# Kernel tuning notes

Hardware: AMD Instinct MI355X
Metric: run time of the kernel (lower is better)

The kernel has to match this reference:

```python
import jax, jax.numpy as jnp
import numpy as np

N_NODES = 100000
N_EDGES = 1600000
F_IN = 64
C = 128          # hidden_encoding == element_embedding
STEPS = 4
NEG_SLOPE = 0.01  # torch.nn.LeakyReLU default


def setup_inputs() -> dict:
    key = jax.random.key(0)
    ks = jax.random.split(key, 8)
    s = 0.05
    return {
        "x": jax.random.normal(ks[0], (N_NODES, F_IN), dtype=jnp.float32),
        "edge_index": jax.random.randint(ks[1], (2, N_EDGES), 0, N_NODES, dtype=jnp.int64),
        "W_in": jax.random.normal(ks[2], (C, F_IN), dtype=jnp.float32) * s,
        "W_mpnn": jax.random.normal(ks[3], (STEPS, C, C), dtype=jnp.float32) * s,
        "W_ih": jax.random.normal(ks[4], (3 * C, C), dtype=jnp.float32) * s,
        "W_hh": jax.random.normal(ks[5], (3 * C, C), dtype=jnp.float32) * s,
        "b_ih": jnp.zeros((3 * C,), dtype=jnp.float32),
        "b_hh": jnp.zeros((3 * C,), dtype=jnp.float32),
        "W_pred": jax.random.normal(ks[6], (1, C), dtype=jnp.float32) * s,
        "b_pred": jnp.zeros((1,), dtype=jnp.float32),
    }


def reference(x, edge_index, W_in, W_mpnn, W_ih, W_hh, b_ih, b_hh, W_pred, b_pred):
    src, dst = edge_index[0], edge_index[1]
    n = x.shape[0]
    # input embedding (bias=False)
    h = x @ W_in.T                                  # [N, C]
    for i in range(STEPS):
        m = h @ W_mpnn[i]                           # [N, C] (PyG: matmul(x, weight[i]))
        agg = jax.ops.segment_sum(m[src], dst, num_segments=n)  # scatter-add aggr
        # torch GRUCell, gate order r, z, n
        gi = agg @ W_ih.T + b_ih                    # [N, 3C]
        gh = h @ W_hh.T + b_hh                      # [N, 3C]
        r = jax.nn.sigmoid(gi[:, :C] + gh[:, :C])
        z = jax.nn.sigmoid(gi[:, C:2 * C] + gh[:, C:2 * C])
        nn_ = jnp.tanh(gi[:, 2 * C:] + r * gh[:, 2 * C:])
        h = (1.0 - z) * nn_ + z * h
    h = jnp.where(h >= 0, h, NEG_SLOPE * h)         # LeakyReLU
    g = jnp.mean(h, axis=0)                         # graph readout [C]
    return g @ W_pred.T + b_pred                    # [1]
```

## Files before the change

### kernel.cpp

```cpp
#include <hip/hip_runtime.h>
#include <cstdint>

typedef __attribute__((ext_vector_type(8))) short bf16x8;
typedef __attribute__((ext_vector_type(4))) float f32x4;
typedef __attribute__((address_space(1))) unsigned int ga_u32;
typedef __attribute__((address_space(3))) unsigned int ls_u32;

__device__ __forceinline__ float bf2f(unsigned short u) {
    union { unsigned int i; float f; } v; v.i = ((unsigned int)u) << 16; return v.f;
}
__device__ __forceinline__ float bfhi(unsigned int w) {
    union { unsigned int i; float f; } v; v.i = w & 0xffff0000u; return v.f;
}
__device__ __forceinline__ float bflo(unsigned int w) {
    union { unsigned int i; float f; } v; v.i = w << 16; return v.f;
}
__device__ __forceinline__ unsigned short f2bf(float f) {
    union { float ff; unsigned int i; } v; v.ff = f;
    unsigned int r = (v.i + 0x7fffu + ((v.i >> 16) & 1u)) >> 16;
    return (unsigned short)r;
}
__device__ __forceinline__ int origcol(int nc) {
    int w = nc / 96, rem = nc % 96, g = rem / 32, cc = rem % 32;
    return g * 128 + w * 32 + cc;
}

__global__ void detect_kernel(const unsigned int* __restrict__ x32,
                              const int* __restrict__ ei32,
                              int* __restrict__ flags)
{
    __shared__ int insaneS;
    __shared__ int orS;
    int tid = threadIdx.x;
    if (tid == 0) { insaneS = 0; orS = 0; }
    __syncthreads();
    int insane = 0;
    for (int j = tid; j < 512; j += 256) {
        unsigned int w = x32[j];
        int e = (int)((w >> 7) & 0xFF);
        if (e > 135 || e < 100) insane++;
    }
    int ov = 0;
    for (int j = tid; j < 256; j += 256) ov |= ei32[2 * j + 1];
    atomicAdd(&insaneS, insane);
    atomicOr(&orS, ov);
    __syncthreads();
    if (tid == 0) {
        flags[0] = (insaneS < 64) ? 1 : 0;
        flags[1] = (orS == 0) ? 1 : 0;
    }
}

__global__ void convall_kernel(const void* W_in, const void* W_mpnn, const void* W_ih,
                               const void* W_hh, const void* b_ih, const void* b_hh,
                               const void* W_pred, const void* b_pred,
                               float* __restrict__ Winf, float* __restrict__ Wmf,
                               float* __restrict__ Wihf, float* __restrict__ Whhf,
                               float* __restrict__ bihf, float* __restrict__ bhhf,
                               float* __restrict__ Wpf, float* __restrict__ bpf,
                               int steps, const int* __restrict__ flags)
{
    int i = blockIdx.x * 256 + threadIdx.x;
    int bf = flags[0];
    auto get = [&](const void* p, int idx) -> float {
        return bf ? bf2f(((const unsigned short*)p)[idx]) : ((const float*)p)[idx];
    };
    int n0 = 8192, n1 = n0 + steps * 16384, n2 = n1 + 49152, n3 = n2 + 49152;
    int n4 = n3 + 384, n5 = n4 + 384, n6 = n5 + 128, n7 = n6 + 1;
    if      (i < n0) Winf[i]      = get(W_in,   i);
    else if (i < n1) Wmf[i - n0]  = get(W_mpnn, i - n0);
    else if (i < n2) Wihf[i - n1] = get(W_ih,   i - n1);
    else if (i < n3) Whhf[i - n2] = get(W_hh,   i - n2);
    else if (i < n4) bihf[i - n3] = get(b_ih,   i - n3);
    else if (i < n5) bhhf[i - n4] = get(b_hh,   i - n4);
    else if (i < n6) Wpf[i - n5]  = get(W_pred, i - n5);
    else if (i < n7) bpf[i - n6]  = get(b_pred, i - n6);
}

__global__ void wcomb_kernel(const float* __restrict__ Wm,
                             const float* __restrict__ Wih,
                             float* __restrict__ Wcomb, int steps)
{
    int i = blockIdx.x * 256 + threadIdx.x;
    int total = steps * 49152;
    if (i >= total) return;
    int step = i / 49152;
    int rem = i - step * 49152;
    int k = rem / 384;
    int j = rem - k * 384;
    const float* wm = Wm + ((long)step * 128 + k) * 128;
    const float* wi = Wih + (long)j * 128;
    float s = 0.f;
#pragma unroll 8
    for (int t = 0; t < 128; ++t) s += wm[t] * wi[t];
    Wcomb[i] = s;
}

__global__ void pack_gates(const float* __restrict__ Wcomb,
                           const float* __restrict__ Whhf,
                           const float* __restrict__ bihf, const float* __restrict__ bhhf,
                           unsigned short* __restrict__ Bci,
                           unsigned short* __restrict__ Bhh,
                           float* __restrict__ bip, float* __restrict__ bhp,
                           int steps)
{
    int i = blockIdx.x * 256 + threadIdx.x;
    int nmat = steps * 49152;
    if (i < nmat) {
        int s = i / 49152, r = i - s * 49152;
        int t = r >> 11, rem = r & 2047;
        int ks = rem >> 9, l = (rem >> 3) & 63, j = rem & 7;
        int k = ks * 32 + (l >> 4) * 8 + j;
        int oc = origcol(t * 16 + (l & 15));
        Bci[i] = f2bf(Wcomb[(long)s * 49152 + k * 384 + oc]);
    } else if (i < nmat + 49152) {
        int r = i - nmat;
        int t = r >> 11, rem = r & 2047;
        int ks = rem >> 9, l = (rem >> 3) & 63, j = rem & 7;
        int k = ks * 32 + (l >> 4) * 8 + j;
        int oc = origcol(t * 16 + (l & 15));
        Bhh[r] = f2bf(Whhf[(long)oc * 128 + k]);
    } else if (i < nmat + 49152 + 768) {
        int b = i - nmat - 49152;
        if (b < 384) bip[b] = bihf[origcol(b)];
        else         bhp[b - 384] = bhhf[origcol(b - 384)];
    }
}

__global__ void pack_in(const float* __restrict__ Winf, unsigned short* __restrict__ Bin)
{
    int r = blockIdx.x * 256 + threadIdx.x;
    if (r >= 8192) return;
    int t = r >> 10, rem = r & 1023;
    int ks = rem >> 9, l = (rem >> 3) & 63, j = rem & 7;
    int k = ks * 32 + (l >> 4) * 8 + j;
    int col = t * 16 + (l & 15);
    Bin[r] = f2bf(Winf[col * 64 + k]);
}

__global__ __launch_bounds__(256) void gemm_in(const void* __restrict__ xraw,
                        const int* __restrict__ flags,
                        const unsigned short* __restrict__ Bin,
                        unsigned short* __restrict__ hout, int N)
{
    const int w = threadIdx.x >> 6, lane = threadIdx.x & 63;
    const int m = lane & 15, quad = lane >> 4;
    const int rowBase = blockIdx.x * 32;
    const bool abf = flags[0] != 0;
    f32x4 acc[2][2];
#pragma unroll
    for (int rt = 0; rt < 2; ++rt)
#pragma unroll
        for (int ct = 0; ct < 2; ++ct) acc[rt][ct] = (f32x4){0.f, 0.f, 0.f, 0.f};

#pragma unroll
    for (int ks = 0; ks < 2; ++ks) {
        bf16x8 a[2];
#pragma unroll
        for (int rt = 0; rt < 2; ++rt) {
            long row = rowBase + rt * 16 + m;
            if (abf) {
                a[rt] = *(const bf16x8*)(const void*)((const unsigned short*)xraw + row * 64 + ks * 32 + quad * 8);
            } else {
                const float* xp = (const float*)xraw + row * 64 + ks * 32 + quad * 8;
                float4 f0 = *(const float4*)xp;
                float4 f1 = *(const float4*)(xp + 4);
                bf16x8 t;
                t[0] = (short)f2bf(f0.x); t[1] = (short)f2bf(f0.y);
                t[2] = (short)f2bf(f0.z); t[3] = (short)f2bf(f0.w);
                t[4] = (short)f2bf(f1.x); t[5] = (short)f2bf(f1.y);
                t[6] = (short)f2bf(f1.z); t[7] = (short)f2bf(f1.w);
                a[rt] = t;
            }
        }
#pragma unroll
        for (int ct = 0; ct < 2; ++ct) {
            int t = w * 2 + ct;
            bf16x8 b = *(const bf16x8*)(const void*)(Bin + ((t * 2 + ks) * 64 + lane) * 8);
#pragma unroll
            for (int rt = 0; rt < 2; ++rt)
                acc[rt][ct] = __builtin_amdgcn_mfma_f32_16x16x32_bf16(a[rt], b, acc[rt][ct], 0, 0, 0);
        }
    }
#pragma unroll
    for (int rt = 0; rt < 2; ++rt)
#pragma unroll
        for (int ct = 0; ct < 2; ++ct)
#pragma unroll
            for (int reg = 0; reg < 4; ++reg) {
                int row = rowBase + rt * 16 + quad * 4 + reg;
                int col = w * 32 + ct * 16 + m;
                if (row < N) hout[(long)row * 128 + col] = f2bf(acc[rt][ct][reg]);
            }
}

__global__ __launch_bounds__(512, 2) void step_kernel(
    const unsigned short* __restrict__ hin,
    const unsigned short* __restrict__ aggb,
    const unsigned short* __restrict__ Bci,
    const unsigned short* __restrict__ Bhh,
    const float* __restrict__ bip, const float* __restrict__ bhp,
    unsigned short* __restrict__ hout, int N)
{
    __shared__ unsigned short lds[8192];
    const int tid = threadIdx.x;
    const int w = tid >> 6, lane = tid & 63;
    const int m = lane & 15, quad = lane >> 4;
    const int cg = w >> 1, half = w & 1;
    const long rowBase = (long)blockIdx.x * 32;
    const int col = cg * 32 + half * 16 + m;

    {
        int lrow = w * 4 + (lane >> 4);
        int schunk = (lane & 15) ^ (lrow & 7);
        const unsigned short* gap = aggb + (rowBase + lrow) * 128 + schunk * 8;
        const unsigned short* ghp = hin  + (rowBase + lrow) * 128 + schunk * 8;
        ls_u32* la = (ls_u32*)(lds + w * 512);
        ls_u32* lh = (ls_u32*)(lds + 4096 + w * 512);
        __builtin_amdgcn_global_load_lds((const ga_u32*)gap, la, 16, 0, 0);
        __builtin_amdgcn_global_load_lds((const ga_u32*)ghp, lh, 16, 0, 0);
    }

    bf16x8 bI[4][3], bH[4][3];
#pragma unroll
    for (int ks = 0; ks < 4; ++ks)
#pragma unroll
        for (int g = 0; g < 3; ++g) {
            int t = cg * 6 + g * 2 + half;
            bI[ks][g] = *(const bf16x8*)(const void*)(Bci + (((long)t * 4 + ks) * 64 + lane) * 8);
            bH[ks][g] = *(const bf16x8*)(const void*)(Bhh + (((long)t * 4 + ks) * 64 + lane) * 8);
        }

    f32x4 gi[2][3], gh[2][3];
#pragma unroll
    for (int g = 0; g < 3; ++g) {
        int nc = (cg * 6 + g * 2 + half) * 16 + m;
        float bi = bip[nc], bh = bhp[nc];
#pragma unroll
        for (int rt = 0; rt < 2; ++rt) {
            gi[rt][g] = (f32x4){bi, bi, bi, bi};
            gh[rt][g] = (f32x4){bh, bh, bh, bh};
        }
    }

    __syncthreads();

#pragma unroll
    for (int ks = 0; ks < 4; ++ks) {
        bf16x8 aA[2], hA[2];
#pragma unroll
        for (int rt = 0; rt < 2; ++rt) {
            int r = rt * 16 + m;
            int ch = (ks * 4 + quad) ^ (r & 7);
            aA[rt] = *(const bf16x8*)(const void*)(lds + r * 128 + ch * 8);
            hA[rt] = *(const bf16x8*)(const void*)(lds + 4096 + r * 128 + ch * 8);
        }
#pragma unroll
        for (int g = 0; g < 3; ++g)
#pragma unroll
            for (int rt = 0; rt < 2; ++rt) {
                gi[rt][g] = __builtin_amdgcn_mfma_f32_16x16x32_bf16(aA[rt], bI[ks][g], gi[rt][g], 0, 0, 0);
                gh[rt][g] = __builtin_amdgcn_mfma_f32_16x16x32_bf16(hA[rt], bH[ks][g], gh[rt][g], 0, 0, 0);
            }
    }

#pragma unroll
    for (int rt = 0; rt < 2; ++rt)
#pragma unroll
        for (int reg = 0; reg < 4; ++reg) {
            long row = rowBase + rt * 16 + quad * 4 + reg;
            if (row < N) {
                int r2 = rt * 16 + quad * 4 + reg;
                int hidx = r2 * 128 + ((((col >> 3) ^ (r2 & 7)) << 3) + (col & 7));
                float R  = __builtin_amdgcn_rcpf(1.f + __expf(-(gi[rt][0][reg] + gh[rt][0][reg])));
                float Z  = __builtin_amdgcn_rcpf(1.f + __expf(-(gi[rt][1][reg] + gh[rt][1][reg])));
                float u  = gi[rt][2][reg] + R * gh[rt][2][reg];
                float e2 = __expf(-2.f * fabsf(u));
                float Nn = copysignf((1.f - e2) * __builtin_amdgcn_rcpf(1.f + e2), u);
                float hold = bf2f(lds[4096 + hidx]);
                hout[row * 128 + col] = f2bf((1.f - Z) * Nn + Z * hold);
            }
        }
}

__global__ __launch_bounds__(256) void part1_kernel(
    const int* __restrict__ ei, int E, const int* __restrict__ flags,
    int* __restrict__ gcnt, uint2* __restrict__ pair2,
    int nb, int cshift, int ccap, int chunk)
{
    __shared__ int cnt[256];
    __shared__ int base_s[256];
    const int tid = threadIdx.x;
    if (tid < nb) cnt[tid] = 0;
    __syncthreads();
    const bool i64 = flags[1] != 0;
    const long long* e64 = (const long long*)ei;
    int lo = blockIdx.x * chunk;
    int hi = lo + chunk; if (hi > E) hi = E;
    for (int i = lo + tid; i < hi; i += 256) {
        int d = i64 ? (int)e64[(long)E + i] : ei[(long)E + i];
        atomicAdd(&cnt[d >> cshift], 1);
    }
    __syncthreads();
    if (tid < nb) {
        int c = cnt[tid];
        base_s[tid] = (c > 0) ? atomicAdd(&gcnt[tid], c) : 0;
        cnt[tid] = 0;
    }
    __syncthreads();
    for (int i = lo + tid; i < hi; i += 256) {
        int s, d;
        if (i64) { s = (int)e64[i]; d = (int)e64[(long)E + i]; }
        else     { s = ei[i];       d = ei[(long)E + i]; }
        int c = d >> cshift;
        int p = base_s[c] + atomicAdd(&cnt[c], 1);
        if (p < ccap) { uint2 pr; pr.x = (unsigned)s; pr.y = (unsigned)d; pair2[(long)c * ccap + p] = pr; }
    }
}

__global__ void scanco_kernel(const int* __restrict__ gcnt, int* __restrict__ cbase,
                              int nb, int ccap)
{
    __shared__ int wsum[4];
    int tid = threadIdx.x, lane = tid & 63, wv = tid >> 6;
    int x = (tid < nb) ? gcnt[tid] : 0;
    if (x > ccap) x = ccap;
    int inc = x;
#pragma unroll
    for (int d = 1; d < 64; d <<= 1) { int u = __shfl_up(inc, d); if (lane >= d) inc += u; }
    if (lane == 63) wsum[wv] = inc;
    __syncthreads();
    if (tid == 0) { int s = 0; for (int q = 0; q < 4; ++q) { int t = wsum[q]; wsum[q] = s; s += t; } }
    __syncthreads();
    int excl = wsum[wv] + inc - x;
    if (tid < nb) cbase[tid] = excl;
    if (tid == nb - 1) cbase[nb] = excl + x;
}

__global__ __launch_bounds__(256) void part2_kernel(
    const uint2* __restrict__ pair2, const int* __restrict__ gcnt,
    const int* __restrict__ cbase,
    int* __restrict__ offs, int* __restrict__ csr,
    int N, int nb, int cshift, int ccap)
{
    __shared__ int lb[2048];
    __shared__ int wsum[4];
    const int b = blockIdx.x, tid = threadIdx.x;
    const int span = 1 << cshift;
    const int n0 = b << cshift;
    int count = gcnt[b]; if (count > ccap) count = ccap;
    for (int k = tid; k < span; k += 256) lb[k] = 0;
    __syncthreads();
    const uint2* pp = pair2 + (long)b * ccap;
    for (int i = tid; i < count; i += 256)
        atomicAdd(&lb[(int)pp[i].y - n0], 1);
    __syncthreads();
    int npe = span >> 8; if (npe < 1) npe = 1;
    int myb = tid * npe;
    int vals[8];
    int sum = 0;
    for (int k = 0; k < npe; ++k) { vals[k] = lb[myb + k]; sum += vals[k]; }
    int lane = tid & 63, wv = tid >> 6;
    int inc = sum;
#pragma unroll
    for (int d = 1; d < 64; d <<= 1) { int u = __shfl_up(inc, d); if (lane >= d) inc += u; }
    if (lane == 63) wsum[wv] = inc;
    __syncthreads();
    if (tid == 0) { int s = 0; for (int q = 0; q < 4; ++q) { int t = wsum[q]; wsum[q] = s; s += t; } }
    __syncthreads();
    int run = wsum[wv] + inc - sum;
    __syncthreads();
    for (int k = 0; k < npe; ++k) { lb[myb + k] = run; run += vals[k]; }
    __syncthreads();
    int gb = cbase[b];
    int nn = N - n0; if (nn > span) nn = span;
    for (int g = tid; g < nn; g += 256) offs[n0 + g] = gb + lb[g];
    if (b == nb - 1 && tid == 0) offs[N] = cbase[nb];
    __syncthreads();
    for (int i = tid; i < count; i += 256) {
        uint2 pr = pp[i];
        int p = gb + atomicAdd(&lb[(int)pr.y - n0], 1);
        csr[p] = (int)pr.x;
    }
}

__global__ __launch_bounds__(256) void aggregate(const unsigned short* __restrict__ hb,
                          const int* __restrict__ off,
                          const int* __restrict__ csr,
                          unsigned short* __restrict__ aggb, int n)
{
    int wv = threadIdx.x >> 6, lane = threadIdx.x & 63;
    int slot = lane >> 4;
    int c16 = lane & 15;
    int nw = gridDim.x * 4;
    int wid = blockIdx.x * 4 + wv;
    int chunk = (n + nw - 1) / nw;
    int lo = wid * chunk;
    int hi = lo + chunk; if (hi > n) hi = n;

    for (int node = lo; node < hi; ++node) {
        int s0 = off[node], s1 = off[node + 1];
        float a0 = 0.f, a1 = 0.f, a2 = 0.f, a3 = 0.f, a4 = 0.f, a5 = 0.f, a6 = 0.f, a7 = 0.f;
        if (s1 > s0) {
            int last = s1 - 1;
            for (int j = s0 + slot; j < s1; j += 16) {
                uint4 vv[4];
                float wt[4];
#pragma unroll
                for (int t = 0; t < 4; ++t) {
                    int jj = j + 4 * t;
                    int idx = csr[jj <= last ? jj : last];
                    vv[t] = *(const uint4*)(const void*)(hb + (long)idx * 128 + c16 * 8);
                    wt[t] = (jj <= last) ? 1.f : 0.f;
                }
#pragma unroll
                for (int t = 0; t < 4; ++t) {
                    a0 = fmaf(bflo(vv[t].x), wt[t], a0);
                    a1 = fmaf(bfhi(vv[t].x), wt[t], a1);
                    a2 = fmaf(bflo(vv[t].y), wt[t], a2);
                    a3 = fmaf(bfhi(vv[t].y), wt[t], a3);
                    a4 = fmaf(bflo(vv[t].z), wt[t], a4);
                    a5 = fmaf(bfhi(vv[t].z), wt[t], a5);
                    a6 = fmaf(bflo(vv[t].w), wt[t], a6);
                    a7 = fmaf(bfhi(vv[t].w), wt[t], a7);
                }
            }
        }
        a0 += __shfl_xor(a0, 16); a1 += __shfl_xor(a1, 16);
        a2 += __shfl_xor(a2, 16); a3 += __shfl_xor(a3, 16);
        a4 += __shfl_xor(a4, 16); a5 += __shfl_xor(a5, 16);
        a6 += __shfl_xor(a6, 16); a7 += __shfl_xor(a7, 16);
        a0 += __shfl_xor(a0, 32); a1 += __shfl_xor(a1, 32);
        a2 += __shfl_xor(a2, 32); a3 += __shfl_xor(a3, 32);
        a4 += __shfl_xor(a4, 32); a5 += __shfl_xor(a5, 32);
        a6 += __shfl_xor(a6, 32); a7 += __shfl_xor(a7, 32);
        if (slot == 0) {
            uint4 o;
            o.x = ((unsigned int)f2bf(a1) << 16) | f2bf(a0);
            o.y = ((unsigned int)f2bf(a3) << 16) | f2bf(a2);
            o.z = ((unsigned int)f2bf(a5) << 16) | f2bf(a4);
            o.w = ((unsigned int)f2bf(a7) << 16) | f2bf(a6);
            *(uint4*)(void*)(aggb + (long)node * 128 + c16 * 8) = o;
        }
    }
}

__global__ void colsum(const unsigned short* __restrict__ hb, float* __restrict__ acc, int n) {
    int c = threadIdx.x & 127;
    int sub = threadIdx.x >> 7;
    float local = 0.f;
    for (long r = blockIdx.x * 2 + sub; r < n; r += (long)gridDim.x * 2) {
        float v = bf2f(hb[r * 128 + c]);
        local += (v >= 0.f) ? v : 0.01f * v;
    }
    atomicAdd(&acc[c], local);
}

__global__ void finalize(const float* __restrict__ acc,
                         const float* __restrict__ W_pred_f,
                         const float* __restrict__ b_pred_f,
                         unsigned int* __restrict__ out, float invN)
{
    __shared__ float ws2[2];
    int t = threadIdx.x;
    float v = acc[t] * invN * W_pred_f[t];
#pragma unroll
    for (int d = 32; d >= 1; d >>= 1) v += __shfl_down(v, d);
    if ((t & 63) == 0) ws2[t >> 6] = v;
    __syncthreads();
    if (t == 0) {
        float r = ws2[0] + ws2[1] + b_pred_f[0];
        unsigned int bf = (unsigned int)f2bf(r);
        out[0] = (bf << 16) | bf;
    }
}

extern "C" void kernel_launch(void* const* d_in, const int* in_sizes, int n_in,
                              void* d_out, int out_size, void* d_ws, size_t ws_size,
                              hipStream_t stream)
{
    const void* x      = d_in[0];
    const int*  ei     = (const int*)d_in[1];
    const void* W_in   = d_in[2];
    const void* W_mpnn = d_in[3];
    const void* W_ih   = d_in[4];
    const void* W_hh   = d_in[5];
    const void* b_ih   = d_in[6];
    const void* b_hh   = d_in[7];
    const void* W_pred = d_in[8];
    const void* b_pred = d_in[9];

    const int N = in_sizes[0] / 64;
    const int E = in_sizes[1] / 2;
    const int STEPS = in_sizes[3] / (128 * 128);

    int cshift = 9;
    while ((((N + (1 << cshift) - 1) >> cshift)) > 256 && cshift < 11) cshift++;
    const int NCO = (N + (1 << cshift) - 1) >> cshift;
    const int ccap = (((E / NCO) * 3 / 2 + 1024) + 255) & ~255;
    const int chunk = (E + 255) / 256;

    size_t woff = 0;
    auto carve = [&](size_t bytes) -> void* {
        void* p = (char*)d_ws + woff;
        woff = (woff + bytes + 255) & ~(size_t)255;
        return p;
    };
    int*   flags = (int*)carve(2 * 4);
    float* Winf  = (float*)carve(8192 * 4);
    float* Wmf   = (float*)carve((size_t)STEPS * 16384 * 4);
    float* Wihf  = (float*)carve(49152 * 4);
    float* Whhf  = (float*)carve(49152 * 4);
    float* bihf  = (float*)carve(384 * 4);
    float* bhhf  = (float*)carve(384 * 4);
    float* Wpf   = (float*)carve(128 * 4);
    float* bpf   = (float*)carve(4);
    float* Wcomb = (float*)carve((size_t)STEPS * 49152 * 4);
    unsigned short* Bci = (unsigned short*)carve((size_t)STEPS * 49152 * 2);
    unsigned short* Bhh = (unsigned short*)carve(49152 * 2);
    unsigned short* Bin = (unsigned short*)carve(8192 * 2);
    float* bip   = (float*)carve(384 * 4);
    float* bhp   = (float*)carve(384 * 4);
    unsigned short* hA   = (unsigned short*)carve(((size_t)N * 128 + 16384) * 2);
    unsigned short* hB   = (unsigned short*)carve(((size_t)N * 128 + 16384) * 2);
    unsigned short* aggb = (unsigned short*)carve(((size_t)N * 128 + 16384) * 2);
    int*   gcnt  = (int*)carve(256 * 4);
    int*   cbase = (int*)carve(257 * 4);
    int*   offs  = (int*)carve((size_t)(N + 1) * 4);
    int*   csr   = (int*)carve((size_t)E * 4 + 256);
    uint2* pair2 = (uint2*)carve((size_t)NCO * ccap * 8);
    float* accb  = (float*)carve(128 * 4);

    hipMemsetAsync(gcnt, 0, 256 * 4, stream);
    hipMemsetAsync(accb, 0, 128 * 4, stream);

    detect_kernel<<<1, 256, 0, stream>>>((const unsigned int*)x, ei, flags);

    {
        int total = 8192 + STEPS * 16384 + 2 * 49152 + 768 + 129;
        convall_kernel<<<(total + 255) / 256, 256, 0, stream>>>(
            W_in, W_mpnn, W_ih, W_hh, b_ih, b_hh, W_pred, b_pred,
            Winf, Wmf, Wihf, Whhf, bihf, bhhf, Wpf, bpf, STEPS, flags);
    }

    wcomb_kernel<<<(STEPS * 49152 + 255) / 256, 256, 0, stream>>>(Wmf, Wihf, Wcomb, STEPS);
    {
        int total = (STEPS + 1) * 49152 + 768;
        pack_gates<<<(total + 255) / 256, 256, 0, stream>>>(Wcomb, Whhf, bihf, bhhf,
                                                            Bci, Bhh, bip, bhp, STEPS);
    }
    pack_in<<<32, 256, 0, stream>>>(Winf, Bin);

    gemm_in<<<(N + 31) / 32, 256, 0, stream>>>(x, flags, Bin, hA, N);

    part1_kernel<<<256, 256, 0, stream>>>(ei, E, flags, gcnt, pair2, NCO, cshift, ccap, chunk);
    scanco_kernel<<<1, 256, 0, stream>>>(gcnt, cbase, NCO, ccap);
    part2_kernel<<<NCO, 256, 0, stream>>>(pair2, gcnt, cbase, offs, csr, N, NCO, cshift, ccap);

    int aggBlocks = (N + 3) / 4; if (aggBlocks > 2048) aggBlocks = 2048;
    unsigned short* hcur = hA;
    unsigned short* hnxt = hB;
    for (int step = 0; step < STEPS; ++step) {
        aggregate<<<aggBlocks, 256, 0, stream>>>(hcur, offs, csr, aggb, N);
        step_kernel<<<(N + 31) / 32, 512, 0, stream>>>(
            hcur, aggb, Bci + (size_t)step * 49152, Bhh, bip, bhp, hnxt, N);
        unsigned short* t = hcur; hcur = hnxt; hnxt = t;
    }

    colsum<<<512, 256, 0, stream>>>(hcur, accb, N);
    finalize<<<1, 128, 0, stream>>>(accb, Wpf, bpf, (unsigned int*)d_out, 1.f / (float)N);
}
```

Measured before the change: 678.4 us.

## Fuse neighbor aggregation into GRU step kernel via LDS staging

Merges the separate aggregate kernel into the per-step GRU kernel. Each 512-thread block gathers and sums neighbor rows for its 32 nodes (4 rows per wave) and writes the bf16 result straight into swizzled LDS, so the aggregate buffer is neither written to nor read back from global memory. This also removes one kernel launch per step. In exchange, the gather work is now split into fixed 32-node tiles with less load balancing, and its latency may not overlap well with the MFMA phase.

```diff
diff --git a/kernel.cpp b/kernel.cpp
--- a/kernel.cpp
+++ b/kernel.cpp
@@ -194,9 +194,10 @@
             }
 }
 
-__global__ __launch_bounds__(512, 2) void step_kernel(
+__global__ __launch_bounds__(512, 2) void fused_step(
     const unsigned short* __restrict__ hin,
-    const unsigned short* __restrict__ aggb,
+    const int* __restrict__ off,
+    const int* __restrict__ csr,
     const unsigned short* __restrict__ Bci,
     const unsigned short* __restrict__ Bhh,
     const float* __restrict__ bip, const float* __restrict__ bhp,
@@ -209,220 +210,48 @@
     const int cg = w >> 1, half = w & 1;
     const long rowBase = (long)blockIdx.x * 32;
     const int col = cg * 32 + half * 16 + m;
+    const int slot = lane >> 4;
+    const int c16 = lane & 15;
 
     {
-        int lrow = w * 4 + (lane >> 4);
-        int schunk = (lane & 15) ^ (lrow & 7);
-        const unsigned short* gap = aggb + (rowBase + lrow) * 128 + schunk * 8;
-        const unsigned short* ghp = hin  + (rowBase + lrow) * 128 + schunk * 8;
-        ls_u32* la = (ls_u32*)(lds + w * 512);
+        int lrow = w * 4 + slot;
+        int schunk = c16 ^ (lrow & 7);
+        const unsigned short* ghp = hin + (rowBase + lrow) * 128 + schunk * 8;
         ls_u32* lh = (ls_u32*)(lds + 4096 + w * 512);
-        __builtin_amdgcn_global_load_lds((const ga_u32*)gap, la, 16, 0, 0);
         __builtin_amdgcn_global_load_lds((const ga_u32*)ghp, lh, 16, 0, 0);
     }
 
-    bf16x8 bI[4][3], bH[4][3];
-#pragma unroll
-    for (int ks = 0; ks < 4; ++ks)
-#pragma unroll
-        for (int g = 0; g < 3; ++g) {
-            int t = cg * 6 + g * 2 + half;
-            bI[ks][g] = *(const bf16x8*)(const void*)(Bci + (((long)t * 4 + ks) * 64 + lane) * 8);
-            bH[ks][g] = *(const bf16x8*)(const void*)(Bhh + (((long)t * 4 + ks) * 64 + lane) * 8);
-        }
-
-    f32x4 gi[2][3], gh[2][3];
-#pragma unroll
-    for (int g = 0; g < 3; ++g) {
-        int nc = (cg * 6 + g * 2 + half) * 16 + m;
-        float bi = bip[nc], bh = bhp[nc];
-#pragma unroll
-        for (int rt = 0; rt < 2; ++rt) {
-            gi[rt][g] = (f32x4){bi, bi, bi, bi};
-            gh[rt][g] = (f32x4){bh, bh, bh, bh};
-        }
-    }
-
-    __syncthreads();
-
-#pragma unroll
-    for (int ks = 0; ks < 4; ++ks) {
-        bf16x8 aA[2], hA[2];
-#pragma unroll
-        for (int rt = 0; rt < 2; ++rt) {
-            int r = rt * 16 + m;
-            int ch = (ks * 4 + quad) ^ (r & 7);
-            aA[rt] = *(const bf16x8*)(const void*)(lds + r * 128 + ch * 8);
-            hA[rt] = *(const bf16x8*)(const void*)(lds + 4096 + r * 128 + ch * 8);
-        }
-#pragma unroll
-        for (int g = 0; g < 3; ++g)
-#pragma unroll
-            for (int rt = 0; rt < 2; ++rt) {
-                gi[rt][g] = __builtin_amdgcn_mfma_f32_16x16x32_bf16(aA[rt], bI[ks][g], gi[rt][g], 0, 0, 0);
-                gh[rt][g] = __builtin_amdgcn_mfma_f32_16x16x32_bf16(hA[rt], bH[ks][g], gh[rt][g], 0, 0, 0);
-            }
-    }
-
-#pragma unroll
-    for (int rt = 0; rt < 2; ++rt)
-#pragma unroll
-        for (int reg = 0; reg < 4; ++reg) {
-            long row = rowBase + rt * 16 + quad * 4 + reg;
-            if (row < N) {
-                int r2 = rt * 16 + quad * 4 + reg;
-                int hidx = r2 * 128 + ((((col >> 3) ^ (r2 & 7)) << 3) + (col & 7));
-                float R  = __builtin_amdgcn_rcpf(1.f + __expf(-(gi[rt][0][reg] + gh[rt][0][reg])));
-                float Z  = __builtin_amdgcn_rcpf(1.f + __expf(-(gi[rt][1][reg] + gh[rt][1][reg])));
-                float u  = gi[rt][2][reg] + R * gh[rt][2][reg];
-                float e2 = __expf(-2.f * fabsf(u));
-                float Nn = copysignf((1.f - e2) * __builtin_amdgcn_rcpf(1.f + e2), u);
-                float hold = bf2f(lds[4096 + hidx]);
-                hout[row * 128 + col] = f2bf((1.f - Z) * Nn + Z * hold);
-            }
-        }
-}
-
-__global__ __launch_bounds__(256) void part1_kernel(
-    const int* __restrict__ ei, int E, const int* __restrict__ flags,
-    int* __restrict__ gcnt, uint2* __restrict__ pair2,
-    int nb, int cshift, int ccap, int chunk)
-{
-    __shared__ int cnt[256];
-    __shared__ int base_s[256];
-    const int tid = threadIdx.x;
-    if (tid < nb) cnt[tid] = 0;
-    __syncthreads();
-    const bool i64 = flags[1] != 0;
-    const long long* e64 = (const long long*)ei;
-    int lo = blockIdx.x * chunk;
-    int hi = lo + chunk; if (hi > E) hi = E;
-    for (int i = lo + tid; i < hi; i += 256) {
-        int d = i64 ? (int)e64[(long)E + i] : ei[(long)E + i];
-        atomicAdd(&cnt[d >> cshift], 1);
-    }
-    __syncthreads();
-    if (tid < nb) {
-        int c = cnt[tid];
-        base_s[tid] = (c > 0) ? atomicAdd(&gcnt[tid], c) : 0;
-        cnt[tid] = 0;
-    }
-    __syncthreads();
-    for (int i = lo + tid; i < hi; i += 256) {
-        int s, d;
-        if (i64) { s = (int)e64[i]; d = (int)e64[(long)E + i]; }
-        else     { s = ei[i];       d = ei[(long)E + i]; }
-        int c = d >> cshift;
-        int p = base_s[c] + atomicAdd(&cnt[c], 1);
-        if (p < ccap) { uint2 pr; pr.x = (unsigned)s; pr.y = (unsigned)d; pair2[(long)c * ccap + p] = pr; }
-    }
-}
-
-__global__ void scanco_kernel(const int* __restrict__ gcnt, int* __restrict__ cbase,
-                              int nb, int ccap)
-{
-    __shared__ int wsum[4];
-    int tid = threadIdx.x, lane = tid & 63, wv = tid >> 6;
-    int x = (tid < nb) ? gcnt[tid] : 0;
-    if (x > ccap) x = ccap;
-    int inc = x;
-#pragma unroll
-    for (int d = 1; d < 64; d <<= 1) { int u = __shfl_up(inc, d); if (lane >= d) inc += u; }
-    if (lane == 63) wsum[wv] = inc;
-    __syncthreads();
-    if (tid == 0) { int s = 0; for (int q = 0; q < 4; ++q) { int t = wsum[q]; wsum[q] = s; s += t; } }
-    __syncthreads();
-    int excl = wsum[wv] + inc - x;
-    if (tid < nb) cbase[tid] = excl;
-    if (tid == nb - 1) cbase[nb] = excl + x;
-}
-
-__global__ __launch_bounds__(256) void part2_kernel(
-    const uint2* __restrict__ pair2, const int* __restrict__ gcnt,
-    const int* __restrict__ cbase,
-    int* __restrict__ offs, int* __restrict__ csr,
-    int N, int nb, int cshift, int ccap)
-{
-    __shared__ int lb[2048];
-    __shared__ int wsum[4];
-    const int b = blockIdx.x, tid = threadIdx.x;
-    const int span = 1 << cshift;
-    const int n0 = b << cshift;
-    int count = gcnt[b]; if (count > ccap) count = ccap;
-    for (int k = tid; k < span; k += 256) lb[k] = 0;
-    __syncthreads();
-    const uint2* pp = pair2 + (long)b * ccap;
-    for (int i = tid; i < count; i += 256)
-        atomicAdd(&lb[(int)pp[i].y - n0], 1);
-    __syncthreads();
-    int npe = span >> 8; if (npe < 1) npe = 1;
-    int myb = tid * npe;
-    int vals[8];
-    int sum = 0;
-    for (int k = 0; k < npe; ++k) { vals[k] = lb[myb + k]; sum += vals[k]; }
-    int lane = tid & 63, wv = tid >> 6;
-    int inc = sum;
-#pragma unroll
-    for (int d = 1; d < 64; d <<= 1) { int u = __shfl_up(inc, d); if (lane >= d) inc += u; }
-    if (lane == 63) wsum[wv] = inc;
-    __syncthreads();
-    if (tid == 0) { int s = 0; for (int q = 0; q < 4; ++q) { int t = wsum[q]; wsum[q] = s; s += t; } }
-    __syncthreads();
-    int run = wsum[wv] + inc - sum;
-    __syncthreads();
-    for (int k = 0; k < npe; ++k) { lb[myb + k] = run; run += vals[k]; }
-    __syncthreads();
-    int gb = cbase[b];
-    int nn = N - n0; if (nn > span) nn = span;
-    for (int g = tid; g < nn; g += 256) offs[n0 + g] = gb + lb[g];
-    if (b == nb - 1 && tid == 0) offs[N] = cbase[nb];
-    __syncthreads();
-    for (int i = tid; i < count; i += 256) {
-        uint2 pr = pp[i];
-        int p = gb + atomicAdd(&lb[(int)pr.y - n0], 1);
-        csr[p] = (int)pr.x;
-    }
-}
-
-__global__ __launch_bounds__(256) void aggregate(const unsigned short* __restrict__ hb,
-                          const int* __restrict__ off,
-                          const int* __restrict__ csr,
-                          unsigned short* __restrict__ aggb, int n)
-{
-    int wv = threadIdx.x >> 6, lane = threadIdx.x & 63;
-    int slot = lane >> 4;
-    int c16 = lane & 15;
-    int nw = gridDim.x * 4;
-    int wid = blockIdx.x * 4 + wv;
-    int chunk = (n + nw - 1) / nw;
-    int lo = wid * chunk;
-    int hi = lo + chunk; if (hi > n) hi = n;
-
-    for (int node = lo; node < hi; ++node) {
-        int s0 = off[node], s1 = off[node + 1];
-        float a0 = 0.f, a1 = 0.f, a2 = 0.f, a3 = 0.f, a4 = 0.f, a5 = 0.f, a6 = 0.f, a7 = 0.f;
-        if (s1 > s0) {
-            int last = s1 - 1;
-            for (int j = s0 + slot; j < s1; j += 16) {
-                uint4 vv[4];
-                float wt[4];
-#pragma unroll
-                for (int t = 0; t < 4; ++t) {
-                    int jj = j + 4 * t;
-                    int idx = csr[jj <= last ? jj : last];
-                    vv[t] = *(const uint4*)(const void*)(hb + (long)idx * 128 + c16 * 8);
-                    wt[t] = (jj <= last) ? 1.f : 0.f;
-                }
-#pragma unroll
-                for (int t = 0; t < 4; ++t) {
-                    a0 = fmaf(bflo(vv[t].x), wt[t], a0);
-                    a1 = fmaf(bfhi(vv[t].x), wt[t], a1);
-                    a2 = fmaf(bflo(vv[t].y), wt[t], a2);
-                    a3 = fmaf(bfhi(vv[t].y), wt[t], a3);
-                    a4 = fmaf(bflo(vv[t].z), wt[t], a4);
-                    a5 = fmaf(bfhi(vv[t].z), wt[t], a5);
-                    a6 = fmaf(bflo(vv[t].w), wt[t], a6);
-                    a7 = fmaf(bfhi(vv[t].w), wt[t], a7);
+#pragma unroll
+    for (int i = 0; i < 4; ++i) {
+        int r = w * 4 + i;
+        long node = rowBase + r;
+        float a0 = 0.f, a1 = 0.f, a2 = 0.f, a3 = 0.f,
+              a4 = 0.f, a5 = 0.f, a6 = 0.f, a7 = 0.f;
+        if (node < N) {
+            int s0 = off[node], s1 = off[node + 1];
+            if (s1 > s0) {
+                int last = s1 - 1;
+                for (int j = s0 + slot; j < s1; j += 16) {
+                    uint4 vv[4];
+                    float wt[4];
+#pragma unroll
+                    for (int t = 0; t < 4; ++t) {
+                        int jj = j + 4 * t;
+                        int idx = csr[jj <= last ? jj : last];
+                        vv[t] = *(const uint4*)(const void*)(hin + (long)idx * 128 + c16 * 8);
+                        wt[t] = (jj <= last) ? 1.f : 0.f;
+                    }
+#pragma unroll
+                    for (int t = 0; t < 4; ++t) {
+                        a0 = fmaf(bflo(vv[t].x), wt[t], a0);
+                        a1 = fmaf(bfhi(vv[t].x), wt[t], a1);
+                        a2 = fmaf(bflo(vv[t].y), wt[t], a2);
+                        a3 = fmaf(bfhi(vv[t].y), wt[t], a3);
+                        a4 = fmaf(bflo(vv[t].z), wt[t], a4);
+                        a5 = fmaf(bfhi(vv[t].z), wt[t], a5);
+                        a6 = fmaf(bflo(vv[t].w), wt[t], a6);
+                        a7 = fmaf(bfhi(vv[t].w), wt[t], a7);
+                    }
                 }
             }
         }
@@ -440,8 +269,170 @@
             o.y = ((unsigned int)f2bf(a3) << 16) | f2bf(a2);
             o.z = ((unsigned int)f2bf(a5) << 16) | f2bf(a4);
             o.w = ((unsigned int)f2bf(a7) << 16) | f2bf(a6);
-            *(uint4*)(void*)(aggb + (long)node * 128 + c16 * 8) = o;
-        }
+            *(uint4*)(void*)(lds + r * 128 + (c16 ^ (r & 7)) * 8) = o;
+        }
+    }
+
+    bf16x8 bI[4][3], bH[4][3];
+#pragma unroll
+    for (int ks = 0; ks < 4; ++ks)
+#pragma unroll
+        for (int g = 0; g < 3; ++g) {
+            int t = cg * 6 + g * 2 + half;
+            bI[ks][g] = *(const bf16x8*)(const void*)(Bci + (((long)t * 4 + ks) * 64 + lane) * 8);
+            bH[ks][g] = *(const bf16x8*)(const void*)(Bhh + (((long)t * 4 + ks) * 64 + lane) * 8);
+        }
+
+    f32x4 gi[2][3], gh[2][3];
+#pragma unroll
+    for (int g = 0; g < 3; ++g) {
+        int nc = (cg * 6 + g * 2 + half) * 16 + m;
+        float bi = bip[nc], bh = bhp[nc];
+#pragma unroll
+        for (int rt = 0; rt < 2; ++rt) {
+            gi[rt][g] = (f32x4){bi, bi, bi, bi};
+            gh[rt][g] = (f32x4){bh, bh, bh, bh};
+        }
+    }
+
+    __syncthreads();
+
+#pragma unroll
+    for (int ks = 0; ks < 4; ++ks) {
+        bf16x8 aA[2], hA[2];
+#pragma unroll
+        for (int rt = 0; rt < 2; ++rt) {
+            int r = rt * 16 + m;
+            int ch = (ks * 4 + quad) ^ (r & 7);
+            aA[rt] = *(const bf16x8*)(const void*)(lds + r * 128 + ch * 8);
+            hA[rt] = *(const bf16x8*)(const void*)(lds + 4096 + r * 128 + ch * 8);
+        }
+#pragma unroll
+        for (int g = 0; g < 3; ++g)
+#pragma unroll
+            for (int rt = 0; rt < 2; ++rt) {
+                gi[rt][g] = __builtin_amdgcn_mfma_f32_16x16x32_bf16(aA[rt], bI[ks][g], gi[rt][g], 0, 0, 0);
+                gh[rt][g] = __builtin_amdgcn_mfma_f32_16x16x32_bf16(hA[rt], bH[ks][g], gh[rt][g], 0, 0, 0);
+            }
+    }
+
+#pragma unroll
+    for (int rt = 0; rt < 2; ++rt)
+#pragma unroll
+        for (int reg = 0; reg < 4; ++reg) {
+            long row = rowBase + rt * 16 + quad * 4 + reg;
+            if (row < N) {
+                int r2 = rt * 16 + quad * 4 + reg;
+                int hidx = r2 * 128 + ((((col >> 3) ^ (r2 & 7)) << 3) + (col & 7));
+                float R  = __builtin_amdgcn_rcpf(1.f + __expf(-(gi[rt][0][reg] + gh[rt][0][reg])));
+                float Z  = __builtin_amdgcn_rcpf(1.f + __expf(-(gi[rt][1][reg] + gh[rt][1][reg])));
+                float u  = gi[rt][2][reg] + R * gh[rt][2][reg];
+                float e2 = __expf(-2.f * fabsf(u));
+                float Nn = copysignf((1.f - e2) * __builtin_amdgcn_rcpf(1.f + e2), u);
+                float hold = bf2f(lds[4096 + hidx]);
+                hout[row * 128 + col] = f2bf((1.f - Z) * Nn + Z * hold);
+            }
+        }
+}
+
+__global__ __launch_bounds__(256) void part1_kernel(
+    const int* __restrict__ ei, int E, const int* __restrict__ flags,
+    int* __restrict__ gcnt, uint2* __restrict__ pair2,
+    int nb, int cshift, int ccap, int chunk)
+{
+    __shared__ int cnt[256];
+    __shared__ int base_s[256];
+    const int tid = threadIdx.x;
+    if (tid < nb) cnt[tid] = 0;
+    __syncthreads();
+    const bool i64 = flags[1] != 0;
+    const long long* e64 = (const long long*)ei;
+    int lo = blockIdx.x * chunk;
+    int hi = lo + chunk; if (hi > E) hi = E;
+    for (int i = lo + tid; i < hi; i += 256) {
+        int d = i64 ? (int)e64[(long)E + i] : ei[(long)E + i];
+        atomicAdd(&cnt[d >> cshift], 1);
+    }
+    __syncthreads();
+    if (tid < nb) {
+        int c = cnt[tid];
+        base_s[tid] = (c > 0) ? atomicAdd(&gcnt[tid], c) : 0;
+        cnt[tid] = 0;
+    }
+    __syncthreads();
+    for (int i = lo + tid; i < hi; i += 256) {
+        int s, d;
+        if (i64) { s = (int)e64[i]; d = (int)e64[(long)E + i]; }
+        else     { s = ei[i];       d = ei[(long)E + i]; }
+        int c = d >> cshift;
+        int p = base_s[c] + atomicAdd(&cnt[c], 1);
+        if (p < ccap) { uint2 pr; pr.x = (unsigned)s; pr.y = (unsigned)d; pair2[(long)c * ccap + p] = pr; }
+    }
+}
+
+__global__ void scanco_kernel(const int* __restrict__ gcnt, int* __restrict__ cbase,
+                              int nb, int ccap)
+{
+    __shared__ int wsum[4];
+    int tid = threadIdx.x, lane = tid & 63, wv = tid >> 6;
+    int x = (tid < nb) ? gcnt[tid] : 0;
+    if (x > ccap) x = ccap;
+    int inc = x;
+#pragma unroll
+    for (int d = 1; d < 64; d <<= 1) { int u = __shfl_up(inc, d); if (lane >= d) inc += u; }
+    if (lane == 63) wsum[wv] = inc;
+    __syncthreads();
+    if (tid == 0) { int s = 0; for (int q = 0; q < 4; ++q) { int t = wsum[q]; wsum[q] = s; s += t; } }
+    __syncthreads();
+    int excl = wsum[wv] + inc - x;
+    if (tid < nb) cbase[tid] = excl;
+    if (tid == nb - 1) cbase[nb] = excl + x;
+}
+
+__global__ __launch_bounds__(256) void part2_kernel(
+    const uint2* __restrict__ pair2, const int* __restrict__ gcnt,
+    const int* __restrict__ cbase,
+    int* __restrict__ offs, int* __restrict__ csr,
+    int N, int nb, int cshift, int ccap)
+{
+    __shared__ int lb[2048];
+    __shared__ int wsum[4];
+    const int b = blockIdx.x, tid = threadIdx.x;
+    const int span = 1 << cshift;
+    const int n0 = b << cshift;
+    int count = gcnt[b]; if (count > ccap) count = ccap;
+    for (int k = tid; k < span; k += 256) lb[k] = 0;
+    __syncthreads();
+    const uint2* pp = pair2 + (long)b * ccap;
+    for (int i = tid; i < count; i += 256)
+        atomicAdd(&lb[(int)pp[i].y - n0], 1);
+    __syncthreads();
+    int npe = span >> 8; if (npe < 1) npe = 1;
+    int myb = tid * npe;
+    int vals[8];
+    int sum = 0;
+    for (int k = 0; k < npe; ++k) { vals[k] = lb[myb + k]; sum += vals[k]; }
+    int lane = tid & 63, wv = tid >> 6;
+    int inc = sum;
+#pragma unroll
+    for (int d = 1; d < 64; d <<= 1) { int u = __shfl_up(inc, d); if (lane >= d) inc += u; }
+    if (lane == 63) wsum[wv] = inc;
+    __syncthreads();
+    if (tid == 0) { int s = 0; for (int q = 0; q < 4; ++q) { int t = wsum[q]; wsum[q] = s; s += t; } }
+    __syncthreads();
+    int run = wsum[wv] + inc - sum;
+    __syncthreads();
+    for (int k = 0; k < npe; ++k) { lb[myb + k] = run; run += vals[k]; }
+    __syncthreads();
+    int gb = cbase[b];
+    int nn = N - n0; if (nn > span) nn = span;
+    for (int g = tid; g < nn; g += 256) offs[n0 + g] = gb + lb[g];
+    if (b == nb - 1 && tid == 0) offs[N] = cbase[nb];
+    __syncthreads();
+    for (int i = tid; i < count; i += 256) {
+        uint2 pr = pp[i];
+        int p = gb + atomicAdd(&lb[(int)pr.y - n0], 1);
+        csr[p] = (int)pr.x;
     }
 }
 
@@ -523,7 +514,6 @@
     float* bhp   = (float*)carve(384 * 4);
     unsigned short* hA   = (unsigned short*)carve(((size_t)N * 128 + 16384) * 2);
     unsigned short* hB   = (unsigned short*)carve(((size_t)N * 128 + 16384) * 2);
-    unsigned short* aggb = (unsigned short*)carve(((size_t)N * 128 + 16384) * 2);
     int*   gcnt  = (int*)carve(256 * 4);
     int*   cbase = (int*)carve(257 * 4);
     int*   offs  = (int*)carve((size_t)(N + 1) * 4);
@@ -557,13 +547,11 @@
     scanco_kernel<<<1, 256, 0, stream>>>(gcnt, cbase, NCO, ccap);
     part2_kernel<<<NCO, 256, 0, stream>>>(pair2, gcnt, cbase, offs, csr, N, NCO, cshift, ccap);
 
-    int aggBlocks = (N + 3) / 4; if (aggBlocks > 2048) aggBlocks = 2048;
     unsigned short* hcur = hA;
     unsigned short* hnxt = hB;
     for (int step = 0; step < STEPS; ++step) {
-        aggregate<<<aggBlocks, 256, 0, stream>>>(hcur, offs, csr, aggb, N);
-        step_kernel<<<(N + 31) / 32, 512, 0, stream>>>(
-            hcur, aggb, Bci + (size_t)step * 49152, Bhh, bip, bhp, hnxt, N);
+        fused_step<<<(N + 31) / 32, 512, 0, stream>>>(
+            hcur, offs, csr, Bci + (size_t)step * 49152, Bhh, bip, bhp, hnxt, N);
         unsigned short* t = hcur; hcur = hnxt; hnxt = t;
     }
 
```

Measured after the change: 765.8 us. 12.9% more time.

## Shrink GRU step tile to 16 rows with 4 waves each owning all gates

Applied to the files above, without the earlier changes.

The step kernel now handles 16 rows per block with 256 threads instead of 32 rows with 512 threads. Each wave owns a 32-column slice for all three gates and both halves, and gate weights are loaded inside the k-loop rather than preloaded into registers. This halves LDS use and register pressure so more blocks fit per CU. The cost is that each block re-reads the full weight set for only 16 rows, doubling total weight traffic through cache and dropping per-wave reuse of B fragments across two row tiles.

```diff
diff --git a/kernel.cpp b/kernel.cpp
--- a/kernel.cpp
+++ b/kernel.cpp
@@ -194,7 +194,7 @@
             }
 }
 
-__global__ __launch_bounds__(512, 2) void step_kernel(
+__global__ __launch_bounds__(256, 4) void step_kernel(
     const unsigned short* __restrict__ hin,
     const unsigned short* __restrict__ aggb,
     const unsigned short* __restrict__ Bci,
@@ -202,82 +202,68 @@
     const float* __restrict__ bip, const float* __restrict__ bhp,
     unsigned short* __restrict__ hout, int N)
 {
-    __shared__ unsigned short lds[8192];
+    __shared__ unsigned short lds[4096];
     const int tid = threadIdx.x;
     const int w = tid >> 6, lane = tid & 63;
     const int m = lane & 15, quad = lane >> 4;
-    const int cg = w >> 1, half = w & 1;
-    const long rowBase = (long)blockIdx.x * 32;
-    const int col = cg * 32 + half * 16 + m;
+    const long rowBase = (long)blockIdx.x * 16;
 
     {
-        int lrow = w * 4 + (lane >> 4);
-        int schunk = (lane & 15) ^ (lrow & 7);
+        int lrow = tid >> 4;
+        int schunk = (tid & 15) ^ (lrow & 7);
         const unsigned short* gap = aggb + (rowBase + lrow) * 128 + schunk * 8;
         const unsigned short* ghp = hin  + (rowBase + lrow) * 128 + schunk * 8;
         ls_u32* la = (ls_u32*)(lds + w * 512);
-        ls_u32* lh = (ls_u32*)(lds + 4096 + w * 512);
+        ls_u32* lh = (ls_u32*)(lds + 2048 + w * 512);
         __builtin_amdgcn_global_load_lds((const ga_u32*)gap, la, 16, 0, 0);
         __builtin_amdgcn_global_load_lds((const ga_u32*)ghp, lh, 16, 0, 0);
     }
 
-    bf16x8 bI[4][3], bH[4][3];
-#pragma unroll
-    for (int ks = 0; ks < 4; ++ks)
-#pragma unroll
-        for (int g = 0; g < 3; ++g) {
-            int t = cg * 6 + g * 2 + half;
-            bI[ks][g] = *(const bf16x8*)(const void*)(Bci + (((long)t * 4 + ks) * 64 + lane) * 8);
-            bH[ks][g] = *(const bf16x8*)(const void*)(Bhh + (((long)t * 4 + ks) * 64 + lane) * 8);
+    f32x4 gi[3][2], gh[3][2];
+#pragma unroll
+    for (int g = 0; g < 3; ++g)
+#pragma unroll
+        for (int half = 0; half < 2; ++half) {
+            int nc = (w * 6 + g * 2 + half) * 16 + m;
+            float bi = bip[nc], bh = bhp[nc];
+            gi[g][half] = (f32x4){bi, bi, bi, bi};
+            gh[g][half] = (f32x4){bh, bh, bh, bh};
         }
 
-    f32x4 gi[2][3], gh[2][3];
-#pragma unroll
-    for (int g = 0; g < 3; ++g) {
-        int nc = (cg * 6 + g * 2 + half) * 16 + m;
-        float bi = bip[nc], bh = bhp[nc];
-#pragma unroll
-        for (int rt = 0; rt < 2; ++rt) {
-            gi[rt][g] = (f32x4){bi, bi, bi, bi};
-            gh[rt][g] = (f32x4){bh, bh, bh, bh};
-        }
-    }
-
     __syncthreads();
 
 #pragma unroll
     for (int ks = 0; ks < 4; ++ks) {
-        bf16x8 aA[2], hA[2];
-#pragma unroll
-        for (int rt = 0; rt < 2; ++rt) {
-            int r = rt * 16 + m;
-            int ch = (ks * 4 + quad) ^ (r & 7);
-            aA[rt] = *(const bf16x8*)(const void*)(lds + r * 128 + ch * 8);
-            hA[rt] = *(const bf16x8*)(const void*)(lds + 4096 + r * 128 + ch * 8);
-        }
+        int ch = (ks * 4 + quad) ^ (m & 7);
+        bf16x8 aA = *(const bf16x8*)(const void*)(lds + m * 128 + ch * 8);
+        bf16x8 hA = *(const bf16x8*)(const void*)(lds + 2048 + m * 128 + ch * 8);
 #pragma unroll
         for (int g = 0; g < 3; ++g)
 #pragma unroll
-            for (int rt = 0; rt < 2; ++rt) {
-                gi[rt][g] = __builtin_amdgcn_mfma_f32_16x16x32_bf16(aA[rt], bI[ks][g], gi[rt][g], 0, 0, 0);
-                gh[rt][g] = __builtin_amdgcn_mfma_f32_16x16x32_bf16(hA[rt], bH[ks][g], gh[rt][g], 0, 0, 0);
+            for (int half = 0; half < 2; ++half) {
+                int t = w * 6 + g * 2 + half;
+                bf16x8 bI = *(const bf16x8*)(const void*)(Bci + (((long)t * 4 + ks) * 64 + lane) * 8);
+                bf16x8 bH = *(const bf16x8*)(const void*)(Bhh + (((long)t * 4 + ks) * 64 + lane) * 8);
+                gi[g][half] = __builtin_amdgcn_mfma_f32_16x16x32_bf16(aA, bI, gi[g][half], 0, 0, 0);
+                gh[g][half] = __builtin_amdgcn_mfma_f32_16x16x32_bf16(hA, bH, gh[g][half], 0, 0, 0);
             }
     }
 
 #pragma unroll
-    for (int rt = 0; rt < 2; ++rt)
+    for (int half = 0; half < 2; ++half)
 #pragma unroll
         for (int reg = 0; reg < 4; ++reg) {
-            long row = rowBase + rt * 16 + quad * 4 + reg;
+            int r2 = quad * 4 + reg;
+            long row = rowBase + r2;
             if (row < N) {
-                int r2 = rt * 16 + quad * 4 + reg;
+                int col = w * 32 + half * 16 + m;
                 int hidx = r2 * 128 + ((((col >> 3) ^ (r2 & 7)) << 3) + (col & 7));
-                float R  = __builtin_amdgcn_rcpf(1.f + __expf(-(gi[rt][0][reg] + gh[rt][0][reg])));
-                float Z  = __builtin_amdgcn_rcpf(1.f + __expf(-(gi[rt][1][reg] + gh[rt][1][reg])));
-                float u  = gi[rt][2][reg] + R * gh[rt][2][reg];
+                float R  = __builtin_amdgcn_rcpf(1.f + __expf(-(gi[0][half][reg] + gh[0][half][reg])));
+                float Z  = __builtin_amdgcn_rcpf(1.f + __expf(-(gi[1][half][reg] + gh[1][half][reg])));
+                float u  = gi[2][half][reg] + R * gh[2][half][reg];
                 float e2 = __expf(-2.f * fabsf(u));
                 float Nn = copysignf((1.f - e2) * __builtin_amdgcn_rcpf(1.f + e2), u);
-                float hold = bf2f(lds[4096 + hidx]);
+                float hold = bf2f(lds[2048 + hidx]);
                 hout[row * 128 + col] = f2bf((1.f - Z) * Nn + Z * hold);
             }
         }
@@ -562,7 +548,7 @@
     unsigned short* hnxt = hB;
     for (int step = 0; step < STEPS; ++step) {
         aggregate<<<aggBlocks, 256, 0, stream>>>(hcur, offs, csr, aggb, N);
-        step_kernel<<<(N + 31) / 32, 512, 0, stream>>>(
+        step_kernel<<<(N + 15) / 16, 256, 0, stream>>>(
             hcur, aggb, Bci + (size_t)step * 49152, Bhh, bip, bhp, hnxt, N);
         unsigned short* t = hcur; hcur = hnxt; hnxt = t;
     }
```

Measured after the change: 691.5 us. Within noise of the previous version (+1.9%).

## Make GRU step kernel persistent with double-buffered LDS prefetch

Applied to the files above, without the earlier changes.

Turns the step kernel into a persistent grid of up to 256 blocks, each looping over 32-row tiles. The next tile's agg and h rows are prefetched into a second LDS buffer with async global-to-LDS loads while the current tile is computed. The gate weight fragments are loaded into registers once per block rather than once per tile. In exchange, LDS use doubles and only 256 blocks run, so the latency hiding that many concurrent blocks gave is lost.

```diff
diff --git a/kernel.cpp b/kernel.cpp
--- a/kernel.cpp
+++ b/kernel.cpp
@@ -200,26 +200,15 @@
     const unsigned short* __restrict__ Bci,
     const unsigned short* __restrict__ Bhh,
     const float* __restrict__ bip, const float* __restrict__ bhp,
-    unsigned short* __restrict__ hout, int N)
-{
-    __shared__ unsigned short lds[8192];
+    unsigned short* __restrict__ hout, int N, int ntiles)
+{
+    __shared__ unsigned short lds[16384];
     const int tid = threadIdx.x;
     const int w = tid >> 6, lane = tid & 63;
     const int m = lane & 15, quad = lane >> 4;
     const int cg = w >> 1, half = w & 1;
-    const long rowBase = (long)blockIdx.x * 32;
     const int col = cg * 32 + half * 16 + m;
-
-    {
-        int lrow = w * 4 + (lane >> 4);
-        int schunk = (lane & 15) ^ (lrow & 7);
-        const unsigned short* gap = aggb + (rowBase + lrow) * 128 + schunk * 8;
-        const unsigned short* ghp = hin  + (rowBase + lrow) * 128 + schunk * 8;
-        ls_u32* la = (ls_u32*)(lds + w * 512);
-        ls_u32* lh = (ls_u32*)(lds + 4096 + w * 512);
-        __builtin_amdgcn_global_load_lds((const ga_u32*)gap, la, 16, 0, 0);
-        __builtin_amdgcn_global_load_lds((const ga_u32*)ghp, lh, 16, 0, 0);
-    }
+    const int grid = gridDim.x;
 
     bf16x8 bI[4][3], bH[4][3];
 #pragma unroll
@@ -230,57 +219,93 @@
             bI[ks][g] = *(const bf16x8*)(const void*)(Bci + (((long)t * 4 + ks) * 64 + lane) * 8);
             bH[ks][g] = *(const bf16x8*)(const void*)(Bhh + (((long)t * 4 + ks) * 64 + lane) * 8);
         }
-
-    f32x4 gi[2][3], gh[2][3];
+    float bi0[3], bh0[3];
 #pragma unroll
     for (int g = 0; g < 3; ++g) {
         int nc = (cg * 6 + g * 2 + half) * 16 + m;
-        float bi = bip[nc], bh = bhp[nc];
-#pragma unroll
-        for (int rt = 0; rt < 2; ++rt) {
-            gi[rt][g] = (f32x4){bi, bi, bi, bi};
-            gh[rt][g] = (f32x4){bh, bh, bh, bh};
-        }
-    }
-
-    __syncthreads();
-
-#pragma unroll
-    for (int ks = 0; ks < 4; ++ks) {
-        bf16x8 aA[2], hA[2];
-#pragma unroll
-        for (int rt = 0; rt < 2; ++rt) {
-            int r = rt * 16 + m;
-            int ch = (ks * 4 + quad) ^ (r & 7);
-            aA[rt] = *(const bf16x8*)(const void*)(lds + r * 128 + ch * 8);
-            hA[rt] = *(const bf16x8*)(const void*)(lds + 4096 + r * 128 + ch * 8);
-        }
+        bi0[g] = bip[nc]; bh0[g] = bhp[nc];
+    }
+
+    const int lrow = w * 4 + (lane >> 4);
+    const int schunk = (lane & 15) ^ (lrow & 7);
+
+    long tile = blockIdx.x;
+    int cur = 0;
+    if (tile < ntiles) {
+        const unsigned short* gap = aggb + (tile * 32 + lrow) * 128 + schunk * 8;
+        const unsigned short* ghp = hin  + (tile * 32 + lrow) * 128 + schunk * 8;
+        __builtin_amdgcn_global_load_lds((const ga_u32*)gap, (ls_u32*)(lds + w * 512), 16, 0, 0);
+        __builtin_amdgcn_global_load_lds((const ga_u32*)ghp, (ls_u32*)(lds + 4096 + w * 512), 16, 0, 0);
+    }
+
+    for (; tile < ntiles; tile += grid) {
+        long nxt = tile + grid;
+        bool hasNext = nxt < ntiles;
+        if (hasNext) {
+            int nb = cur ^ 1;
+            const unsigned short* gap = aggb + (nxt * 32 + lrow) * 128 + schunk * 8;
+            const unsigned short* ghp = hin  + (nxt * 32 + lrow) * 128 + schunk * 8;
+            __builtin_amdgcn_global_load_lds((const ga_u32*)gap, (ls_u32*)(lds + nb * 8192 + w * 512), 16, 0, 0);
+            __builtin_amdgcn_global_load_lds((const ga_u32*)ghp, (ls_u32*)(lds + nb * 8192 + 4096 + w * 512), 16, 0, 0);
+            asm volatile("s_waitcnt vmcnt(2)" ::: "memory");
+        } else {
+            asm volatile("s_waitcnt vmcnt(0)" ::: "memory");
+        }
+        __builtin_amdgcn_s_barrier();
+
+        const unsigned short* abuf = lds + cur * 8192;
+        const unsigned short* hbuf = lds + cur * 8192 + 4096;
+
+        f32x4 gi[2][3], gh[2][3];
 #pragma unroll
         for (int g = 0; g < 3; ++g)
 #pragma unroll
             for (int rt = 0; rt < 2; ++rt) {
-                gi[rt][g] = __builtin_amdgcn_mfma_f32_16x16x32_bf16(aA[rt], bI[ks][g], gi[rt][g], 0, 0, 0);
-                gh[rt][g] = __builtin_amdgcn_mfma_f32_16x16x32_bf16(hA[rt], bH[ks][g], gh[rt][g], 0, 0, 0);
+                gi[rt][g] = (f32x4){bi0[g], bi0[g], bi0[g], bi0[g]};
+                gh[rt][g] = (f32x4){bh0[g], bh0[g], bh0[g], bh0[g]};
             }
-    }
-
-#pragma unroll
-    for (int rt = 0; rt < 2; ++rt)
-#pragma unroll
-        for (int reg = 0; reg < 4; ++reg) {
-            long row = rowBase + rt * 16 + quad * 4 + reg;
-            if (row < N) {
-                int r2 = rt * 16 + quad * 4 + reg;
-                int hidx = r2 * 128 + ((((col >> 3) ^ (r2 & 7)) << 3) + (col & 7));
-                float R  = __builtin_amdgcn_rcpf(1.f + __expf(-(gi[rt][0][reg] + gh[rt][0][reg])));
-                float Z  = __builtin_amdgcn_rcpf(1.f + __expf(-(gi[rt][1][reg] + gh[rt][1][reg])));
-                float u  = gi[rt][2][reg] + R * gh[rt][2][reg];
-                float e2 = __expf(-2.f * fabsf(u));
-                float Nn = copysignf((1.f - e2) * __builtin_amdgcn_rcpf(1.f + e2), u);
-                float hold = bf2f(lds[4096 + hidx]);
-                hout[row * 128 + col] = f2bf((1.f - Z) * Nn + Z * hold);
+
+#pragma unroll
+        for (int ks = 0; ks < 4; ++ks) {
+            bf16x8 aA[2], hA[2];
+#pragma unroll
+            for (int rt = 0; rt < 2; ++rt) {
+                int r = rt * 16 + m;
+                int ch = (ks * 4 + quad) ^ (r & 7);
+                aA[rt] = *(const bf16x8*)(const void*)(abuf + r * 128 + ch * 8);
+                hA[rt] = *(const bf16x8*)(const void*)(hbuf + r * 128 + ch * 8);
             }
-        }
+#pragma unroll
+            for (int g = 0; g < 3; ++g)
+#pragma unroll
+                for (int rt = 0; rt < 2; ++rt) {
+                    gi[rt][g] = __builtin_amdgcn_mfma_f32_16x16x32_bf16(aA[rt], bI[ks][g], gi[rt][g], 0, 0, 0);
+                    gh[rt][g] = __builtin_amdgcn_mfma_f32_16x16x32_bf16(hA[rt], bH[ks][g], gh[rt][g], 0, 0, 0);
+                }
+        }
+
+        long rowBase = tile * 32;
+#pragma unroll
+        for (int rt = 0; rt < 2; ++rt)
+#pragma unroll
+            for (int reg = 0; reg < 4; ++reg) {
+                long row = rowBase + rt * 16 + quad * 4 + reg;
+                if (row < N) {
+                    int r2 = rt * 16 + quad * 4 + reg;
+                    int hidx = r2 * 128 + ((((col >> 3) ^ (r2 & 7)) << 3) + (col & 7));
+                    float R  = __builtin_amdgcn_rcpf(1.f + __expf(-(gi[rt][0][reg] + gh[rt][0][reg])));
+                    float Z  = __builtin_amdgcn_rcpf(1.f + __expf(-(gi[rt][1][reg] + gh[rt][1][reg])));
+                    float u  = gi[rt][2][reg] + R * gh[rt][2][reg];
+                    float e2 = __expf(-2.f * fabsf(u));
+                    float Nn = copysignf((1.f - e2) * __builtin_amdgcn_rcpf(1.f + e2), u);
+                    float hold = bf2f(hbuf[hidx]);
+                    hout[row * 128 + col] = f2bf((1.f - Z) * Nn + Z * hold);
+                }
+            }
+
+        __builtin_amdgcn_s_barrier();
+        cur ^= 1;
+    }
 }
 
 __global__ __launch_bounds__(256) void part1_kernel(
@@ -558,12 +583,14 @@
     part2_kernel<<<NCO, 256, 0, stream>>>(pair2, gcnt, cbase, offs, csr, N, NCO, cshift, ccap);
 
     int aggBlocks = (N + 3) / 4; if (aggBlocks > 2048) aggBlocks = 2048;
+    const int ntiles = (N + 31) / 32;
+    int stepBlocks = ntiles < 256 ? ntiles : 256;
     unsigned short* hcur = hA;
     unsigned short* hnxt = hB;
     for (int step = 0; step < STEPS; ++step) {
         aggregate<<<aggBlocks, 256, 0, stream>>>(hcur, offs, csr, aggb, N);
-        step_kernel<<<(N + 31) / 32, 512, 0, stream>>>(
-            hcur, aggb, Bci + (size_t)step * 49152, Bhh, bip, bhp, hnxt, N);
+        step_kernel<<<stepBlocks, 512, 0, stream>>>(
+            hcur, aggb, Bci + (size_t)step * 49152, Bhh, bip, bhp, hnxt, N, ntiles);
         unsigned short* t = hcur; hcur = hnxt; hnxt = t;
     }
 
```

Result: faster. 595.5 us (-12.2%).
